# Performance work log

Hardware: AMD Instinct MI355X
Metric: run time of the kernel (lower is better)

Reference implementation:

```python
import jax, jax.numpy as jnp
import numpy as np

B, T, N, D = 4, 16, 1024, 128
LN_EPS = 1e-5


def setup_inputs() -> dict:
    key = jax.random.key(0)
    k1, k2, k3 = jax.random.split(key, 3)
    X = jax.random.normal(k1, (B, T, N, D), dtype=jnp.float32)
    # normalized adjacency (dense, values in [0,1))
    A = jax.random.uniform(k2, (N, N), dtype=jnp.float32)
    # GCN linear weight (torch nn.Linear, bias=False): out = x @ W.T
    W = jax.random.normal(k3, (D, D), dtype=jnp.float32) / np.sqrt(D)
    gamma = jnp.ones((D,), dtype=jnp.float32)
    beta = jnp.zeros((D,), dtype=jnp.float32)
    return {"X": X, "A": A, "W": W, "gamma": gamma, "beta": beta}


def reference(X, A, W, gamma, beta):
    d = X.shape[-1]
    inv_sqrt_d_a = np.float32(1.0 / np.sqrt(d + 1e-8))  # score scale
    inv_sqrt_d_b = np.float32(1.0 / np.sqrt(d + 1e-9))  # output scale
    # dynamic attention-like scores over nodes: (b,T,N,N)
    scores = jnp.einsum('btnd,btmd->btnm', X, X)
    St = jax.nn.softmax(scores, axis=-1) * inv_sqrt_d_a  # dropout p=0 => identity
    Aeff = A * St                                        # adjacency-masked attention
    # GCN: relu((Aeff @ X) @ W.T)
    h = jnp.einsum('btnm,btmd->btnd', Aeff, X)
    h = jax.nn.relu(h @ W.T) * inv_sqrt_d_b
    # LayerNorm over last dim
    mu = jnp.mean(h, axis=-1, keepdims=True)
    var = jnp.mean(jnp.square(h - mu), axis=-1, keepdims=True)
    h = (h - mu) * jax.lax.rsqrt(var + LN_EPS) * gamma + beta
    # residual
    return h + X
```

## Files before the change

### kernel.cpp

```cpp
#include <hip/hip_runtime.h>
#include <hip/hip_bf16.h>


#define NNODES 1024
#define DDIM   128
#define BROWS  128
#define WROWS  16
#define MC     64
#define NCHUNK (NNODES / MC)
#define THREADS 512

#define CA 0.08838834764831845f
#define CB 0.08838834764831845f
#define LN_EPS 1e-5f

typedef __attribute__((ext_vector_type(8))) short bf16x8;
typedef __attribute__((ext_vector_type(4))) float f32x4;
typedef __attribute__((ext_vector_type(2))) unsigned int u32x2;

#define STILE(s) (64*(s))

#define XB0_OFF 0
#define XB1_OFF 8192
#define P_OFF   16384
#define P_S     72
#define H_S     136
#define SM_TOT  25600

#define TRREAD8(T0,T1,T2,T3,T4,T5,T6,T7, AP)                                \
  asm volatile(                                                             \
    "ds_read_b64_tr_b16 %0, %8 offset:0\n\t"                                \
    "ds_read_b64_tr_b16 %1, %8 offset:128\n\t"                              \
    "ds_read_b64_tr_b16 %2, %8 offset:2048\n\t"                             \
    "ds_read_b64_tr_b16 %3, %8 offset:2176\n\t"                             \
    "ds_read_b64_tr_b16 %4, %8 offset:4096\n\t"                             \
    "ds_read_b64_tr_b16 %5, %8 offset:4224\n\t"                             \
    "ds_read_b64_tr_b16 %6, %8 offset:6144\n\t"                             \
    "ds_read_b64_tr_b16 %7, %8 offset:6272\n\t"                             \
    "s_waitcnt lgkmcnt(0)"                                                  \
    : "=&v"(T0), "=&v"(T1), "=&v"(T2), "=&v"(T3),                           \
      "=&v"(T4), "=&v"(T5), "=&v"(T6), "=&v"(T7)                            \
    : "v"(AP))

__device__ __forceinline__ unsigned int pk2(float lo, float hi) {
  union { __hip_bfloat162 b2; unsigned int u; } cv;
  cv.b2 = __float22bfloat162_rn(make_float2(lo, hi));
  return cv.u;
}

__device__ __forceinline__ unsigned short f2bf(float f) {
  unsigned int u = __float_as_uint(f);
  u += 0x7FFFu + ((u >> 16) & 1u);
  return (unsigned short)(u >> 16);
}

__device__ __forceinline__ bf16x8 pack8(float4 a, float4 b) {
  union { unsigned int w[4]; bf16x8 v; } u;
  u.w[0] = pk2(a.x, a.y); u.w[1] = pk2(a.z, a.w);
  u.w[2] = pk2(b.x, b.y); u.w[3] = pk2(b.z, b.w);
  return u.v;
}

__device__ __forceinline__ bf16x8 joinpair(u32x2 lo, u32x2 hi) {
  union { u32x2 d[2]; bf16x8 v; } u;
  u.d[0] = lo; u.d[1] = hi;
  return u.v;
}

__global__ __launch_bounds__(THREADS, 4)
void sdgcn_fused(const float* __restrict__ X, const float* __restrict__ A,
                 const float* __restrict__ W, const float* __restrict__ gamma,
                 const float* __restrict__ beta, float* __restrict__ Out) {
  const int bt   = blockIdx.x;
  const int row0 = blockIdx.y * BROWS;
  const int tid  = (int)threadIdx.x;
  const int wid  = tid >> 6;
  const int lane = tid & 63;
  const int c    = lane & 15;
  const int q    = lane >> 4;
  const int c2 = c >> 2, c3 = c & 3, q1 = q & 1, q2 = q >> 1;

  const float* Xbt = X + (size_t)bt * NNODES * DDIM;

  __shared__ __align__(128) unsigned short sm[SM_TOT];
  unsigned short* Pw = sm + P_OFF + wid * (WROWS * P_S);

  const int pswz = 16 * ((c >> 3) & 1);

  bf16x8 qfrag[4];
  float ss = 0.f;
  {
    const float* qrow = Xbt + (size_t)(row0 + wid * WROWS + c) * DDIM;
#pragma unroll
    for (int ds = 0; ds < 4; ++ds) {
      const float* p = qrow + ds * 32 + q * 8;
      float4 a = *(const float4*)p;
      float4 b = *(const float4*)(p + 4);
      ss += a.x*a.x + a.y*a.y + a.z*a.z + a.w*a.w;
      ss += b.x*b.x + b.y*b.y + b.z*b.z + b.w*b.w;
      qfrag[ds] = pack8(a, b);
    }
    ss += __shfl_xor(ss, 16, 64);
    ss += __shfl_xor(ss, 32, 64);
  }

  float z_acc = 0.f;
  f32x4 Ofr[8];
#pragma unroll
  for (int dt = 0; dt < 8; ++dt) Ofr[dt] = (f32x4){0.f, 0.f, 0.f, 0.f};

  const int grow = row0 + wid * WROWS + q * 4;
  const int arow = row0 + wid * WROWS + c;

  const int h4  = tid & 15;
  const int mlo = (tid >> 4) & 3;
  const int sd4 = h4 + 16 * (wid & 1);
  const int mh0 = wid >> 1;
  const int sst = (sd4 >> 2) * 16 + mh0;
  const int sof = 16*mlo + 4*(sd4 & 3);

  {
    float4 stg[4];
#pragma unroll
    for (int k = 0; k < 4; ++k)
      stg[k] = *(const float4*)(Xbt + (size_t)(mlo + 4*(mh0 + 4*k)) * DDIM + sd4 * 4);
#pragma unroll
    for (int k = 0; k < 4; ++k) {
      float4 v = stg[k];
      *(uint2*)(sm + XB0_OFF + STILE(sst + 4*k) + sof) =
          make_uint2(pk2(v.x, v.y), pk2(v.z, v.w));
    }
  }

  for (int ch = 0; ch < NCHUNK; ++ch) {
    const int m0 = ch * MC;
    unsigned short* xb  = sm + ((ch & 1) ? XB1_OFF : XB0_OFF);
    unsigned short* xbn = sm + ((ch & 1) ? XB0_OFF : XB1_OFF);
    const unsigned trb = (unsigned)(size_t)xb + 256u*q + 8u*c;

    __syncthreads();

    float4 stg[4];
    if (ch + 1 < NCHUNK) {
      const float* nx = Xbt + (size_t)(m0 + MC) * DDIM;
#pragma unroll
      for (int k = 0; k < 4; ++k)
        stg[k] = *(const float4*)(nx + (size_t)(mlo + 4*(mh0 + 4*k)) * DDIM + sd4 * 4);
    }
    float4 av[4];
#pragma unroll
    for (int mt = 0; mt < 4; ++mt)
      av[mt] = *(const float4*)(A + (size_t)arow * NNODES + m0 + mt*16 + 4*q);
    f32x4 S[4];
#pragma unroll
    for (int mt = 0; mt < 4; ++mt) {
      f32x4 acc = (f32x4){0.f, 0.f, 0.f, 0.f};
#pragma unroll
      for (int ds = 0; ds < 4; ++ds) {
        const bf16x8 bf = *(const bf16x8*)(xb + STILE((ds*2 + q2)*16 + mt*4 + c2)
                                              + 16*c3 + 8*q1);
        acc = __builtin_amdgcn_mfma_f32_16x16x32_bf16(bf, qfrag[ds], acc, 0, 0, 0);
      }
      S[mt] = acc;
    }
    if (ch + 1 < NCHUNK) {
#pragma unroll
      for (int k = 0; k < 4; ++k) {
        float4 v = stg[k];
        *(uint2*)(xbn + STILE(sst + 4*k) + sof) =
            make_uint2(pk2(v.x, v.y), pk2(v.z, v.w));
      }
    }
    float zr = 0.f;
#pragma unroll
    for (int mt = 0; mt < 4; ++mt) {
      float p0 = __expf(S[mt][0] - ss);
      float p1 = __expf(S[mt][1] - ss);
      float p2 = __expf(S[mt][2] - ss);
      float p3 = __expf(S[mt][3] - ss);
      zr += (p0 + p1) + (p2 + p3);
      *(uint2*)(Pw + c * P_S + ((mt*16 + 4*q) ^ pswz)) =
          make_uint2(pk2(p0 * av[mt].x, p1 * av[mt].y),
                     pk2(p2 * av[mt].z, p3 * av[mt].w));
    }
    z_acc += zr;
#pragma unroll
    for (int ks = 0; ks < 2; ++ks) {
      const bf16x8 pf = *(const bf16x8*)(Pw + c * P_S + ((ks*32 + q*8) ^ pswz));
      u32x2 t0, t1, t2, t3, t4, t5, t6, t7;
      TRREAD8(t0, t1, t2, t3, t4, t5, t6, t7, trb + 1024u*ks);
      Ofr[0] = __builtin_amdgcn_mfma_f32_16x16x32_bf16(pf, joinpair(t0, t1), Ofr[0], 0, 0, 0);
      Ofr[1] = __builtin_amdgcn_mfma_f32_16x16x32_bf16(pf, joinpair(t2, t3), Ofr[1], 0, 0, 0);
      Ofr[2] = __builtin_amdgcn_mfma_f32_16x16x32_bf16(pf, joinpair(t4, t5), Ofr[2], 0, 0, 0);
      Ofr[3] = __builtin_amdgcn_mfma_f32_16x16x32_bf16(pf, joinpair(t6, t7), Ofr[3], 0, 0, 0);
      TRREAD8(t0, t1, t2, t3, t4, t5, t6, t7, trb + 1024u*ks + 8192u);
      Ofr[4] = __builtin_amdgcn_mfma_f32_16x16x32_bf16(pf, joinpair(t0, t1), Ofr[4], 0, 0, 0);
      Ofr[5] = __builtin_amdgcn_mfma_f32_16x16x32_bf16(pf, joinpair(t2, t3), Ofr[5], 0, 0, 0);
      Ofr[6] = __builtin_amdgcn_mfma_f32_16x16x32_bf16(pf, joinpair(t4, t5), Ofr[6], 0, 0, 0);
      Ofr[7] = __builtin_amdgcn_mfma_f32_16x16x32_bf16(pf, joinpair(t6, t7), Ofr[7], 0, 0, 0);
    }
  }

  z_acc += __shfl_xor(z_acc, 16, 64);
  z_acc += __shfl_xor(z_acc, 32, 64);
  float zrow[4];
#pragma unroll
  for (int r = 0; r < 4; ++r)
    zrow[r] = __shfl(z_acc, (lane & 48) + ((lane & 48) >> 2) + r, 64);

  __syncthreads();
  unsigned short* Hw = sm + wid * (WROWS * H_S);
#pragma unroll
  for (int r = 0; r < 4; ++r) {
    float rinv = CA / zrow[r];
#pragma unroll
    for (int dt = 0; dt < 8; ++dt)
      Hw[(q*4 + r) * H_S + (((dt*16) ^ (16*(q>>1))) + c)] = f2bf(Ofr[dt][r] * rinv);
  }
  f32x4 G[8];
#pragma unroll
  for (int jt = 0; jt < 8; ++jt) G[jt] = (f32x4){0.f, 0.f, 0.f, 0.f};
#pragma unroll
  for (int ks = 0; ks < 4; ++ks) {
    bf16x8 hf = *(const bf16x8*)(Hw + c * H_S + ((ks*32 + q*8) ^ pswz));
#pragma unroll
    for (int jt = 0; jt < 8; ++jt) {
      const float* wr = W + (size_t)(jt*16 + c) * DDIM + ks*32 + q*8;
      float4 a = *(const float4*)wr;
      float4 b = *(const float4*)(wr + 4);
      bf16x8 wf = pack8(a, b);
      G[jt] = __builtin_amdgcn_mfma_f32_16x16x32_bf16(hf, wf, G[jt], 0, 0, 0);
    }
  }
#pragma unroll
  for (int jt = 0; jt < 8; ++jt) {
#pragma unroll
    for (int r = 0; r < 4; ++r) G[jt][r] = fmaxf(G[jt][r], 0.f) * CB;
  }
  float* Obt = Out + (size_t)bt * NNODES * DDIM;
#pragma unroll
  for (int r = 0; r < 4; ++r) {
    float s1 = 0.f, s2 = 0.f;
#pragma unroll
    for (int jt = 0; jt < 8; ++jt) { float v = G[jt][r]; s1 += v; s2 += v * v; }
#pragma unroll
    for (int off = 1; off < 16; off <<= 1) {
      s1 += __shfl_xor(s1, off, 64);
      s2 += __shfl_xor(s2, off, 64);
    }
    float mu = s1 * (1.f / 128.f);
    float va = s2 * (1.f / 128.f) - mu * mu;
    float rs = rsqrtf(va + LN_EPS);
    const float* xr = Xbt + (size_t)(grow + r) * DDIM;
    float* orow = Obt + (size_t)(grow + r) * DDIM;
#pragma unroll
    for (int jt = 0; jt < 8; ++jt) {
      int col = jt * 16 + c;
      orow[col] = (G[jt][r] - mu) * rs * gamma[col] + beta[col] + xr[col];
    }
  }
}

extern "C" void kernel_launch(void* const* d_in, const int* in_sizes, int n_in,
                              void* d_out, int out_size, void* d_ws, size_t ws_size,
                              hipStream_t stream) {
  const float* X     = (const float*)d_in[0];
  const float* A     = (const float*)d_in[1];
  const float* W     = (const float*)d_in[2];
  const float* gamma = (const float*)d_in[3];
  const float* beta  = (const float*)d_in[4];
  float* Out = (float*)d_out;
  dim3 grid(64, NNODES / BROWS);
  hipLaunchKernelGGL(sdgcn_fused, grid, dim3(THREADS), 0, stream, X, A, W, gamma, beta, Out);
}
```

Baseline: 173.5 us.

## Halve block rows to 64 with 4 waves and split X staging into two phases

Each block now owns 64 node rows and runs 4 waves (256 threads) instead of 128 rows and 8 waves, which doubles the grid and shrinks shared memory per block. Each thread therefore stages twice as many X rows per chunk. That staging is split into two batches of four loads, one stored after the score MFMAs and one after the softmax, to keep register pressure low while the global loads overlap compute. The cost is that every block re-reads and converts the full X tile, so global traffic and conversion work per output row go up.

```diff
diff --git a/kernel.cpp b/kernel.cpp
--- a/kernel.cpp
+++ b/kernel.cpp
@@ -4,11 +4,12 @@
 
 #define NNODES 1024
 #define DDIM   128
-#define BROWS  128
+#define BROWS  64
 #define WROWS  16
+#define NWAVES 4
 #define MC     64
 #define NCHUNK (NNODES / MC)
-#define THREADS 512
+#define THREADS 256
 
 #define CA 0.08838834764831845f
 #define CB 0.08838834764831845f
@@ -25,7 +26,7 @@
 #define P_OFF   16384
 #define P_S     72
 #define H_S     136
-#define SM_TOT  25600
+#define SM_TOT  20992
 
 #define TRREAD8(T0,T1,T2,T3,T4,T5,T6,T7, AP)                                \
   asm volatile(                                                             \
@@ -116,18 +117,14 @@
   const int mlo = (tid >> 4) & 3;
   const int sd4 = h4 + 16 * (wid & 1);
   const int mh0 = wid >> 1;
-  const int sst = (sd4 >> 2) * 16 + mh0;
   const int sof = 16*mlo + 4*(sd4 & 3);
+  const int scl = (sd4 >> 2) * 16;
 
   {
-    float4 stg[4];
-#pragma unroll
-    for (int k = 0; k < 4; ++k)
-      stg[k] = *(const float4*)(Xbt + (size_t)(mlo + 4*(mh0 + 4*k)) * DDIM + sd4 * 4);
-#pragma unroll
-    for (int k = 0; k < 4; ++k) {
-      float4 v = stg[k];
-      *(uint2*)(sm + XB0_OFF + STILE(sst + 4*k) + sof) =
+#pragma unroll
+    for (int k = 0; k < 8; ++k) {
+      float4 v = *(const float4*)(Xbt + (size_t)(mlo + 4*(mh0 + 2*k)) * DDIM + sd4 * 4);
+      *(uint2*)(sm + XB0_OFF + STILE(scl + mh0 + 2*k) + sof) =
           make_uint2(pk2(v.x, v.y), pk2(v.z, v.w));
     }
   }
@@ -140,12 +137,14 @@
 
     __syncthreads();
 
-    float4 stg[4];
-    if (ch + 1 < NCHUNK) {
-      const float* nx = Xbt + (size_t)(m0 + MC) * DDIM;
-#pragma unroll
-      for (int k = 0; k < 4; ++k)
-        stg[k] = *(const float4*)(nx + (size_t)(mlo + 4*(mh0 + 4*k)) * DDIM + sd4 * 4);
+    const bool pre = (ch + 1 < NCHUNK);
+    const float* nx = Xbt + (size_t)(m0 + MC) * DDIM;
+    float4 sA0, sA1, sA2, sA3;
+    if (pre) {
+      sA0 = *(const float4*)(nx + (size_t)(mlo + 4*(mh0 + 0)) * DDIM + sd4 * 4);
+      sA1 = *(const float4*)(nx + (size_t)(mlo + 4*(mh0 + 2)) * DDIM + sd4 * 4);
+      sA2 = *(const float4*)(nx + (size_t)(mlo + 4*(mh0 + 4)) * DDIM + sd4 * 4);
+      sA3 = *(const float4*)(nx + (size_t)(mlo + 4*(mh0 + 6)) * DDIM + sd4 * 4);
     }
     float4 av[4];
 #pragma unroll
@@ -163,13 +162,16 @@
       }
       S[mt] = acc;
     }
-    if (ch + 1 < NCHUNK) {
-#pragma unroll
-      for (int k = 0; k < 4; ++k) {
-        float4 v = stg[k];
-        *(uint2*)(xbn + STILE(sst + 4*k) + sof) =
-            make_uint2(pk2(v.x, v.y), pk2(v.z, v.w));
-      }
+    float4 sB0, sB1, sB2, sB3;
+    if (pre) {
+      *(uint2*)(xbn + STILE(scl + mh0 + 0) + sof) = make_uint2(pk2(sA0.x, sA0.y), pk2(sA0.z, sA0.w));
+      *(uint2*)(xbn + STILE(scl + mh0 + 2) + sof) = make_uint2(pk2(sA1.x, sA1.y), pk2(sA1.z, sA1.w));
+      *(uint2*)(xbn + STILE(scl + mh0 + 4) + sof) = make_uint2(pk2(sA2.x, sA2.y), pk2(sA2.z, sA2.w));
+      *(uint2*)(xbn + STILE(scl + mh0 + 6) + sof) = make_uint2(pk2(sA3.x, sA3.y), pk2(sA3.z, sA3.w));
+      sB0 = *(const float4*)(nx + (size_t)(mlo + 4*(mh0 +  8)) * DDIM + sd4 * 4);
+      sB1 = *(const float4*)(nx + (size_t)(mlo + 4*(mh0 + 10)) * DDIM + sd4 * 4);
+      sB2 = *(const float4*)(nx + (size_t)(mlo + 4*(mh0 + 12)) * DDIM + sd4 * 4);
+      sB3 = *(const float4*)(nx + (size_t)(mlo + 4*(mh0 + 14)) * DDIM + sd4 * 4);
     }
     float zr = 0.f;
 #pragma unroll
@@ -184,6 +186,12 @@
                      pk2(p2 * av[mt].z, p3 * av[mt].w));
     }
     z_acc += zr;
+    if (pre) {
+      *(uint2*)(xbn + STILE(scl + mh0 +  8) + sof) = make_uint2(pk2(sB0.x, sB0.y), pk2(sB0.z, sB0.w));
+      *(uint2*)(xbn + STILE(scl + mh0 + 10) + sof) = make_uint2(pk2(sB1.x, sB1.y), pk2(sB1.z, sB1.w));
+      *(uint2*)(xbn + STILE(scl + mh0 + 12) + sof) = make_uint2(pk2(sB2.x, sB2.y), pk2(sB2.z, sB2.w));
+      *(uint2*)(xbn + STILE(scl + mh0 + 14) + sof) = make_uint2(pk2(sB3.x, sB3.y), pk2(sB3.z, sB3.w));
+    }
 #pragma unroll
     for (int ks = 0; ks < 2; ++ks) {
       const bf16x8 pf = *(const bf16x8*)(Pw + c * P_S + ((ks*32 + q*8) ^ pswz));
```

After: 236.1 us. +36.1%, slower.

## Software-pipeline PV matmul one chunk behind QK with triple-buffered X tiles

Applied to the files above, without the earlier changes.

Moves the P·X MFMA step so each iteration runs it for the previous chunk while computing scores for the current chunk, using a three-slot X buffer in shared memory. The adjacency loads are moved after the score MFMAs. The goal is to overlap the softmax and exp work with the PV matrix multiply and hide LDS/global latency. The cost is more shared memory, and the occupancy hint drops from 4 to 2 blocks per CU.

```diff
diff --git a/kernel.cpp b/kernel.cpp
--- a/kernel.cpp
+++ b/kernel.cpp
@@ -20,12 +20,11 @@
 
 #define STILE(s) (64*(s))
 
-#define XB0_OFF 0
-#define XB1_OFF 8192
-#define P_OFF   16384
+#define XB_STR  8192
+#define P_OFF   24576
 #define P_S     72
 #define H_S     136
-#define SM_TOT  25600
+#define SM_TOT  33792
 
 #define TRREAD8(T0,T1,T2,T3,T4,T5,T6,T7, AP)                                \
   asm volatile(                                                             \
@@ -42,6 +41,26 @@
       "=&v"(T4), "=&v"(T5), "=&v"(T6), "=&v"(T7)                            \
     : "v"(AP))
 
+#define PV_STEP(XBP)                                                        \
+  do {                                                                      \
+    const unsigned trb_ = (unsigned)(size_t)(XBP) + 256u*q + 8u*c;          \
+    _Pragma("unroll")                                                       \
+    for (int ks = 0; ks < 2; ++ks) {                                        \
+      const bf16x8 pf = *(const bf16x8*)(Pw + c * P_S + ((ks*32 + q*8) ^ pswz)); \
+      u32x2 t0, t1, t2, t3, t4, t5, t6, t7;                                 \
+      TRREAD8(t0, t1, t2, t3, t4, t5, t6, t7, trb_ + 1024u*ks);             \
+      Ofr[0] = __builtin_amdgcn_mfma_f32_16x16x32_bf16(pf, joinpair(t0, t1), Ofr[0], 0, 0, 0); \
+      Ofr[1] = __builtin_amdgcn_mfma_f32_16x16x32_bf16(pf, joinpair(t2, t3), Ofr[1], 0, 0, 0); \
+      Ofr[2] = __builtin_amdgcn_mfma_f32_16x16x32_bf16(pf, joinpair(t4, t5), Ofr[2], 0, 0, 0); \
+      Ofr[3] = __builtin_amdgcn_mfma_f32_16x16x32_bf16(pf, joinpair(t6, t7), Ofr[3], 0, 0, 0); \
+      TRREAD8(t0, t1, t2, t3, t4, t5, t6, t7, trb_ + 1024u*ks + 8192u);     \
+      Ofr[4] = __builtin_amdgcn_mfma_f32_16x16x32_bf16(pf, joinpair(t0, t1), Ofr[4], 0, 0, 0); \
+      Ofr[5] = __builtin_amdgcn_mfma_f32_16x16x32_bf16(pf, joinpair(t2, t3), Ofr[5], 0, 0, 0); \
+      Ofr[6] = __builtin_amdgcn_mfma_f32_16x16x32_bf16(pf, joinpair(t4, t5), Ofr[6], 0, 0, 0); \
+      Ofr[7] = __builtin_amdgcn_mfma_f32_16x16x32_bf16(pf, joinpair(t6, t7), Ofr[7], 0, 0, 0); \
+    }                                                                       \
+  } while (0)
+
 __device__ __forceinline__ unsigned int pk2(float lo, float hi) {
   union { __hip_bfloat162 b2; unsigned int u; } cv;
   cv.b2 = __float22bfloat162_rn(make_float2(lo, hi));
@@ -67,7 +86,7 @@
   return u.v;
 }
 
-__global__ __launch_bounds__(THREADS, 4)
+__global__ __launch_bounds__(THREADS, 2)
 void sdgcn_fused(const float* __restrict__ X, const float* __restrict__ A,
                  const float* __restrict__ W, const float* __restrict__ gamma,
                  const float* __restrict__ beta, float* __restrict__ Out) {
@@ -127,16 +146,16 @@
 #pragma unroll
     for (int k = 0; k < 4; ++k) {
       float4 v = stg[k];
-      *(uint2*)(sm + XB0_OFF + STILE(sst + 4*k) + sof) =
+      *(uint2*)(sm + STILE(sst + 4*k) + sof) =
           make_uint2(pk2(v.x, v.y), pk2(v.z, v.w));
     }
   }
 
   for (int ch = 0; ch < NCHUNK; ++ch) {
     const int m0 = ch * MC;
-    unsigned short* xb  = sm + ((ch & 1) ? XB1_OFF : XB0_OFF);
-    unsigned short* xbn = sm + ((ch & 1) ? XB0_OFF : XB1_OFF);
-    const unsigned trb = (unsigned)(size_t)xb + 256u*q + 8u*c;
+    unsigned short* xb_c = sm + XB_STR * (ch % 3);
+    unsigned short* xb_n = sm + XB_STR * ((ch + 1) % 3);
+    unsigned short* xb_p = sm + XB_STR * ((ch + 2) % 3);
 
     __syncthreads();
 
@@ -147,18 +166,14 @@
       for (int k = 0; k < 4; ++k)
         stg[k] = *(const float4*)(nx + (size_t)(mlo + 4*(mh0 + 4*k)) * DDIM + sd4 * 4);
     }
-    float4 av[4];
-#pragma unroll
-    for (int mt = 0; mt < 4; ++mt)
-      av[mt] = *(const float4*)(A + (size_t)arow * NNODES + m0 + mt*16 + 4*q);
     f32x4 S[4];
 #pragma unroll
     for (int mt = 0; mt < 4; ++mt) {
       f32x4 acc = (f32x4){0.f, 0.f, 0.f, 0.f};
 #pragma unroll
       for (int ds = 0; ds < 4; ++ds) {
-        const bf16x8 bf = *(const bf16x8*)(xb + STILE((ds*2 + q2)*16 + mt*4 + c2)
-                                              + 16*c3 + 8*q1);
+        const bf16x8 bf = *(const bf16x8*)(xb_c + STILE((ds*2 + q2)*16 + mt*4 + c2)
+                                                + 16*c3 + 8*q1);
         acc = __builtin_amdgcn_mfma_f32_16x16x32_bf16(bf, qfrag[ds], acc, 0, 0, 0);
       }
       S[mt] = acc;
@@ -167,10 +182,15 @@
 #pragma unroll
       for (int k = 0; k < 4; ++k) {
         float4 v = stg[k];
-        *(uint2*)(xbn + STILE(sst + 4*k) + sof) =
+        *(uint2*)(xb_n + STILE(sst + 4*k) + sof) =
             make_uint2(pk2(v.x, v.y), pk2(v.z, v.w));
       }
     }
+    float4 av[4];
+#pragma unroll
+    for (int mt = 0; mt < 4; ++mt)
+      av[mt] = *(const float4*)(A + (size_t)arow * NNODES + m0 + mt*16 + 4*q);
+    if (ch > 0) PV_STEP(xb_p);
     float zr = 0.f;
 #pragma unroll
     for (int mt = 0; mt < 4; ++mt) {
@@ -184,22 +204,8 @@
                      pk2(p2 * av[mt].z, p3 * av[mt].w));
     }
     z_acc += zr;
-#pragma unroll
-    for (int ks = 0; ks < 2; ++ks) {
-      const bf16x8 pf = *(const bf16x8*)(Pw + c * P_S + ((ks*32 + q*8) ^ pswz));
-      u32x2 t0, t1, t2, t3, t4, t5, t6, t7;
-      TRREAD8(t0, t1, t2, t3, t4, t5, t6, t7, trb + 1024u*ks);
-      Ofr[0] = __builtin_amdgcn_mfma_f32_16x16x32_bf16(pf, joinpair(t0, t1), Ofr[0], 0, 0, 0);
-      Ofr[1] = __builtin_amdgcn_mfma_f32_16x16x32_bf16(pf, joinpair(t2, t3), Ofr[1], 0, 0, 0);
-      Ofr[2] = __builtin_amdgcn_mfma_f32_16x16x32_bf16(pf, joinpair(t4, t5), Ofr[2], 0, 0, 0);
-      Ofr[3] = __builtin_amdgcn_mfma_f32_16x16x32_bf16(pf, joinpair(t6, t7), Ofr[3], 0, 0, 0);
-      TRREAD8(t0, t1, t2, t3, t4, t5, t6, t7, trb + 1024u*ks + 8192u);
-      Ofr[4] = __builtin_amdgcn_mfma_f32_16x16x32_bf16(pf, joinpair(t0, t1), Ofr[4], 0, 0, 0);
-      Ofr[5] = __builtin_amdgcn_mfma_f32_16x16x32_bf16(pf, joinpair(t2, t3), Ofr[5], 0, 0, 0);
-      Ofr[6] = __builtin_amdgcn_mfma_f32_16x16x32_bf16(pf, joinpair(t4, t5), Ofr[6], 0, 0, 0);
-      Ofr[7] = __builtin_amdgcn_mfma_f32_16x16x32_bf16(pf, joinpair(t6, t7), Ofr[7], 0, 0, 0);
-    }
-  }
+  }
+  PV_STEP(sm + XB_STR * ((NCHUNK - 1) % 3));
 
   z_acc += __shfl_xor(z_acc, 16, 64);
   z_acc += __shfl_xor(z_acc, 32, 64);
```

Result: no change. 175.4 us (+1.1%).
